# Performance work log

Hardware: AMD Instinct MI355X
Metric: run time of the kernel (lower is better)

The kernel has to match this reference:

```python
import jax, jax.numpy as jnp
import numpy as np

N_STATE = 1024
N_HEAD = 16
B = 2
S = 2048


def setup_inputs() -> dict:
    key = jax.random.key(0)
    ks = jax.random.split(key, 8)
    s = 0.02
    x = jax.random.normal(ks[0], (B, S, N_STATE), dtype=jnp.float32)
    # causal additive mask, as in Whisper: upper triangle = -inf
    mask = jnp.where(jnp.triu(jnp.ones((S, S), dtype=bool), k=1), -jnp.inf, 0.0).astype(jnp.float32)
    Wq = jax.random.normal(ks[1], (N_STATE, N_STATE), dtype=jnp.float32) * s
    bq = jax.random.normal(ks[2], (N_STATE,), dtype=jnp.float32) * s
    Wk = jax.random.normal(ks[3], (N_STATE, N_STATE), dtype=jnp.float32) * s
    Wv = jax.random.normal(ks[4], (N_STATE, N_STATE), dtype=jnp.float32) * s
    bv = jax.random.normal(ks[5], (N_STATE,), dtype=jnp.float32) * s
    Wo = jax.random.normal(ks[6], (N_STATE, N_STATE), dtype=jnp.float32) * s
    bo = jax.random.normal(ks[7], (N_STATE,), dtype=jnp.float32) * s
    return {"x": x, "mask": mask, "Wq": Wq, "bq": bq, "Wk": Wk,
            "Wv": Wv, "bv": bv, "Wo": Wo, "bo": bo}


def reference(x, mask, Wq, bq, Wk, Wv, bv, Wo, bo):
    Bb, S_, D = x.shape
    H = N_HEAD
    hd = D // H
    scale = hd ** (-0.25)  # scale split across q and k, as in the source
    q = x @ Wq.T + bq              # [B,S,D]
    k = x @ Wk.T                   # key has no bias
    v = x @ Wv.T + bv
    # [B,S,D] -> [B,H,S,hd]
    q = q.reshape(Bb, S_, H, hd).transpose(0, 2, 1, 3) * scale
    k = k.reshape(Bb, S_, H, hd).transpose(0, 2, 1, 3) * scale
    v = v.reshape(Bb, S_, H, hd).transpose(0, 2, 1, 3)
    qk = jnp.einsum('bhsd,bhtd->bhst', q, k) + mask[:S_, :S_]
    w = jax.nn.softmax(qk, axis=-1).astype(q.dtype)
    out = jnp.einsum('bhst,bhtd->bhsd', w, v)
    out = out.transpose(0, 2, 1, 3).reshape(Bb, S_, D)
    return out @ Wo.T + bo
```

## Files before the change

kernel.cpp:

```cpp
#include <hip/hip_runtime.h>
#include <hip/hip_bf16.h>
#include <cmath>

typedef __bf16 bf16;
typedef __bf16 bf16x8 __attribute__((ext_vector_type(8)));
typedef __bf16 bf16x4 __attribute__((ext_vector_type(4)));
typedef float f32x4 __attribute__((ext_vector_type(4)));

#define QS 0.18033688f

__device__ __forceinline__ void load16_to_lds(const void* g, void* l) {
    __builtin_amdgcn_global_load_lds(
        (const __attribute__((address_space(1))) unsigned int*)g,
        (__attribute__((address_space(3))) unsigned int*)l, 16, 0, 0);
}

__global__ __launch_bounds__(256) void convert_kernel(
    const float* __restrict__ x,  const float* __restrict__ wq,
    const float* __restrict__ wk, const float* __restrict__ wv,
    const float* __restrict__ wo, bf16* __restrict__ dst)
{
    const size_t M1 = 1024ull * 1024ull, M4 = 4ull * M1;
    size_t i0 = ((size_t)blockIdx.x * 256 + threadIdx.x) * 8;
    const float* s;
    size_t off;
    float sc = 1.f;
    if      (i0 < M4)        { s = x;  off = i0; }
    else if (i0 < M4 + M1)   { s = wq; off = i0 - M4; sc = QS; }
    else if (i0 < M4 + 2*M1) { s = wk; off = i0 - M4 - M1; }
    else if (i0 < M4 + 3*M1) { s = wv; off = i0 - M4 - 2*M1; }
    else                     { s = wo; off = i0 - M4 - 3*M1; }
    float4 a = *(const float4*)(s + off);
    float4 b = *(const float4*)(s + off + 4);
    bf16x8 r = { (bf16)(a.x*sc), (bf16)(a.y*sc), (bf16)(a.z*sc), (bf16)(a.w*sc),
                 (bf16)(b.x*sc), (bf16)(b.y*sc), (bf16)(b.z*sc), (bf16)(b.w*sc) };
    *(bf16x8*)(dst + i0) = r;
}

template<int BM, int MODE>
__device__ __forceinline__ void gemm_core(
    const bf16* __restrict__ A, const bf16* __restrict__ W,
    const float* __restrict__ bias, void* __restrict__ C,
    int mb, int nb, float bias_scale)
{
    constexpr int IF = BM / 32;
    __shared__ __align__(16) bf16 As[BM * 32];
    __shared__ __align__(16) bf16 Bs[128 * 32];

    const int tid  = threadIdx.x;
    const int lane = tid & 63;
    const int wave = tid >> 6;
    const int wr   = (wave >> 1) * (BM / 2);
    const int wc   = (wave & 1) * 64;
    const int l15  = lane & 15;
    const int l4   = lane >> 4;
    const int swz  = (l4 ^ ((l15 >> 1) & 3)) * 8;

    f32x4 acc[IF][4] = {};

    for (int kt = 0; kt < 32; ++kt) {
#pragma unroll
        for (int it = 0; it < BM / 64; ++it) {
            int c = it * 256 + tid;
            int scol = ((c & 3) ^ ((c >> 3) & 3)) * 8;
            load16_to_lds(&A[(size_t)(mb * BM + (c >> 2)) * 1024 + kt * 32 + scol],
                          &As[(it * 256 + (tid & 192)) * 8]);
        }
#pragma unroll
        for (int it = 0; it < 2; ++it) {
            int c = it * 256 + tid;
            int scol = ((c & 3) ^ ((c >> 3) & 3)) * 8;
            load16_to_lds(&W[(size_t)(nb * 128 + (c >> 2)) * 1024 + kt * 32 + scol],
                          &Bs[(it * 256 + (tid & 192)) * 8]);
        }
        __syncthreads();
        bf16x8 af[IF], bfr[4];
#pragma unroll
        for (int i = 0; i < IF; ++i)
            af[i] = *(const bf16x8*)&As[(wr + i * 16 + l15) * 32 + swz];
#pragma unroll
        for (int j = 0; j < 4; ++j)
            bfr[j] = *(const bf16x8*)&Bs[(wc + j * 16 + l15) * 32 + swz];
#pragma unroll
        for (int i = 0; i < IF; ++i)
#pragma unroll
            for (int j = 0; j < 4; ++j)
                acc[i][j] = __builtin_amdgcn_mfma_f32_16x16x32_bf16(
                    af[i], bfr[j], acc[i][j], 0, 0, 0);
        __syncthreads();
    }

    if (MODE == 1 || MODE == 2) {
#pragma unroll
        for (int j = 0; j < 4; ++j) {
            int D = nb * 128 + wc + j * 16 + l15;
            float bv = bias ? bias[D] : 0.f;
            int hh = D >> 6, d = D & 63;
#pragma unroll
            for (int i = 0; i < IF; ++i) {
                int S0 = mb * BM + wr + i * 16 + l4 * 4;
#pragma unroll
                for (int r = 0; r < 4; ++r) {
                    int S = S0 + r;
                    int bb = S >> 11, key = S & 2047;
                    int bh = bb * 16 + hh, nt = key >> 6, ktl = key & 63;
                    size_t idx;
                    if (MODE == 1)
                        idx = ((size_t)(bh * 32 + nt) * 8 + (d >> 5) * 4 + (ktl >> 4)) * 512
                            + ((d >> 3) & 3) * 128 + (ktl & 15) * 8 + (d & 7);
                    else
                        idx = ((size_t)(bh * 32 + nt) * 8 + (ktl >> 5) * 4 + (d >> 4)) * 512
                            + ((ktl >> 3) & 3) * 128 + (d & 15) * 8 + (ktl & 7);
                    ((bf16*)C)[idx] = (bf16)(acc[i][j][r] + bv);
                }
            }
        }
    } else {
#pragma unroll
        for (int j = 0; j < 4; ++j) {
            int col = nb * 128 + wc + j * 16 + l15;
            float bv = bias ? bias[col] * bias_scale : 0.f;
#pragma unroll
            for (int i = 0; i < IF; ++i) {
                int row0 = mb * BM + wr + i * 16 + l4 * 4;
#pragma unroll
                for (int r = 0; r < 4; ++r) {
                    float val = acc[i][j][r] + bv;
                    size_t idx = (size_t)(row0 + r) * 1024 + col;
                    if (MODE == 3) ((float*)C)[idx] = val;
                    else           ((bf16*)C)[idx]  = (bf16)val;
                }
            }
        }
    }
}

__global__ __launch_bounds__(256) void qkv_kernel(
    const bf16* __restrict__ xb,
    const bf16* __restrict__ wqb, const float* __restrict__ bq,
    const bf16* __restrict__ wkb,
    const bf16* __restrict__ wvb, const float* __restrict__ bv,
    bf16* __restrict__ q, bf16* __restrict__ kfb, bf16* __restrict__ vfb)
{
    int mb = blockIdx.x;
    int nbg = blockIdx.y;
    int sel = nbg >> 3, nb = nbg & 7;
    if      (sel == 0) gemm_core<128, 0>(xb, wqb, bq,      q,   mb, nb, QS);
    else if (sel == 1) gemm_core<128, 1>(xb, wkb, nullptr, kfb, mb, nb, 1.f);
    else               gemm_core<128, 2>(xb, wvb, bv,      vfb, mb, nb, 1.f);
}

__global__ __launch_bounds__(256) void oproj_kernel(
    const bf16* __restrict__ ao, const bf16* __restrict__ wob,
    const float* __restrict__ bo, float* __restrict__ out)
{
    gemm_core<128, 3>(ao, wob, bo, out, blockIdx.x, blockIdx.y, 1.f);
}

__global__ __launch_bounds__(64, 4) void attn_kernel(
    const bf16* __restrict__ q, const bf16* __restrict__ kfb,
    const bf16* __restrict__ vfb, bf16* __restrict__ o)
{
    __shared__ __align__(16) bf16 Ps[32 * 72];

    const int lane = threadIdx.x;
    const int l15  = lane & 15;
    const int l4   = lane >> 4;

    const int bh = blockIdx.x;
    const int wt = 63 - blockIdx.y;
    const int b  = bh >> 4, h = bh & 15;
    const int qrow0 = wt * 32;

    bf16x8 qf[2][2];
#pragma unroll
    for (int qb = 0; qb < 2; ++qb)
#pragma unroll
        for (int kk = 0; kk < 2; ++kk)
            qf[qb][kk] = *(const bf16x8*)&q[(size_t)(b * 2048 + qrow0 + qb * 16 + l15) * 1024
                                           + h * 64 + kk * 32 + l4 * 8];

    const bf16* kb = kfb + (size_t)bh * 131072;
    const bf16* vb = vfb + (size_t)bh * 131072;

    f32x4 oacc[2][4] = {};
    float lsum[2] = { 0.f, 0.f };

    const int n = (qrow0 >> 6) + 1;
    for (int nt = 0; nt < n; ++nt) {
        const bf16* kt_ = kb + nt * 4096;
        const bf16* vt_ = vb + nt * 4096;

        f32x4 s[2][4] = {};
#pragma unroll
        for (int kk = 0; kk < 2; ++kk) {
#pragma unroll
            for (int j = 0; j < 4; ++j) {
                bf16x8 kf = *(const bf16x8*)&kt_[(kk * 4 + j) * 512 + lane * 8];
                s[0][j] = __builtin_amdgcn_mfma_f32_16x16x32_bf16(kf, qf[0][kk], s[0][j], 0, 0, 0);
                s[1][j] = __builtin_amdgcn_mfma_f32_16x16x32_bf16(kf, qf[1][kk], s[1][j], 0, 0, 0);
            }
        }

        const bool diag = (nt == n - 1);
#pragma unroll
        for (int qb = 0; qb < 2; ++qb) {
            float pv[4][4];
            if (diag) {
                int qg = qrow0 + qb * 16 + l15;
#pragma unroll
                for (int j = 0; j < 4; ++j)
#pragma unroll
                    for (int r = 0; r < 4; ++r) {
                        int kg = nt * 64 + j * 16 + l4 * 4 + r;
                        pv[j][r] = (kg > qg) ? 0.f : __builtin_amdgcn_exp2f(s[qb][j][r]);
                    }
            } else {
#pragma unroll
                for (int j = 0; j < 4; ++j)
#pragma unroll
                    for (int r = 0; r < 4; ++r)
                        pv[j][r] = __builtin_amdgcn_exp2f(s[qb][j][r]);
            }
#pragma unroll
            for (int j = 0; j < 4; ++j)
                lsum[qb] += (pv[j][0] + pv[j][1]) + (pv[j][2] + pv[j][3]);

#pragma unroll
            for (int j = 0; j < 4; ++j) {
                bf16x4 pk = { (bf16)pv[j][0], (bf16)pv[j][1], (bf16)pv[j][2], (bf16)pv[j][3] };
                *(bf16x4*)&Ps[(qb * 16 + l15) * 72 + j * 16 + l4 * 4] = pk;
            }
        }

#pragma unroll
        for (int kk = 0; kk < 2; ++kk) {
            bf16x8 pf0 = *(const bf16x8*)&Ps[l15 * 72 + kk * 32 + l4 * 8];
            bf16x8 pf1 = *(const bf16x8*)&Ps[(16 + l15) * 72 + kk * 32 + l4 * 8];
#pragma unroll
            for (int f = 0; f < 4; ++f) {
                bf16x8 vf = *(const bf16x8*)&vt_[(kk * 4 + f) * 512 + lane * 8];
                oacc[0][f] = __builtin_amdgcn_mfma_f32_16x16x32_bf16(pf0, vf, oacc[0][f], 0, 0, 0);
                oacc[1][f] = __builtin_amdgcn_mfma_f32_16x16x32_bf16(pf1, vf, oacc[1][f], 0, 0, 0);
            }
        }
    }

#pragma unroll
    for (int qb = 0; qb < 2; ++qb) {
        float ls = lsum[qb];
        ls += __shfl_xor(ls, 16, 64);
        ls += __shfl_xor(ls, 32, 64);
        float rinv[4];
#pragma unroll
        for (int r = 0; r < 4; ++r) rinv[r] = 1.f / __shfl(ls, l4 * 4 + r, 64);
#pragma unroll
        for (int f = 0; f < 4; ++f)
#pragma unroll
            for (int r = 0; r < 4; ++r)
                o[(size_t)(b * 2048 + qrow0 + qb * 16 + l4 * 4 + r) * 1024 + h * 64 + f * 16 + l15]
                    = (bf16)(oacc[qb][f][r] * rinv[r]);
    }
}

extern "C" void kernel_launch(void* const* d_in, const int* in_sizes, int n_in,
                              void* d_out, int out_size, void* d_ws, size_t ws_size,
                              hipStream_t stream)
{
    const float* x  = (const float*)d_in[0];
    const float* Wq = (const float*)d_in[2];
    const float* bq = (const float*)d_in[3];
    const float* Wk = (const float*)d_in[4];
    const float* Wv = (const float*)d_in[5];
    const float* bv = (const float*)d_in[6];
    const float* Wo = (const float*)d_in[7];
    const float* bo = (const float*)d_in[8];
    float* out = (float*)d_out;

    const size_t M1 = 1024ull * 1024ull, M4 = 4ull * M1;
    bf16* base = (bf16*)d_ws;
    bf16* xb  = base;
    bf16* wqb = base + M4;
    bf16* wkb = base + M4 + M1;
    bf16* wvb = base + M4 + 2 * M1;
    bf16* wob = base + M4 + 3 * M1;
    bf16* q   = base + 8 * M1;
    bf16* kfb = base + 12 * M1;
    bf16* vfb = base + 16 * M1;
    bf16* ao  = xb;

    convert_kernel<<<4096, 256, 0, stream>>>(x, Wq, Wk, Wv, Wo, base);
    qkv_kernel<<<dim3(32, 24), 256, 0, stream>>>(xb, wqb, bq, wkb, wvb, bv, q, kfb, vfb);
    attn_kernel<<<dim3(32, 64), 64, 0, stream>>>(q, kfb, vfb, ao);
    oproj_kernel<<<dim3(32, 8), 256, 0, stream>>>(ao, wob, bo, out);
}
```

Baseline: 195.2 us.

## Split causal attention KV loop into chunks and add a combine kernel

The attention kernel gains a third grid dimension that splits each query tile's KV loop into chunks of up to 8 tiles. Chunk partial outputs and row sums go to an fp32 workspace buffer, and a new combine kernel sums them and normalizes. Tiles with only one chunk still write their output directly. The aim is to even out the causal workload imbalance and shorten the tail of long query tiles, at the cost of an extra launch, partial-result memory traffic, and many empty early-exit blocks.

```diff
diff --git a/kernel.cpp b/kernel.cpp
--- a/kernel.cpp
+++ b/kernel.cpp
@@ -159,7 +159,8 @@
 
 __global__ __launch_bounds__(64, 4) void attn_kernel(
     const bf16* __restrict__ q, const bf16* __restrict__ kfb,
-    const bf16* __restrict__ vfb, bf16* __restrict__ o)
+    const bf16* __restrict__ vfb, bf16* __restrict__ o,
+    float* __restrict__ pbuf)
 {
     __shared__ __align__(16) bf16 Ps[32 * 72];
 
@@ -167,10 +168,17 @@
     const int l15  = lane & 15;
     const int l4   = lane >> 4;
 
-    const int bh = blockIdx.x;
-    const int wt = 63 - blockIdx.y;
+    const int bh    = blockIdx.x;
+    const int wt    = 63 - blockIdx.y;
+    const int chunk = blockIdx.z;
     const int b  = bh >> 4, h = bh & 15;
     const int qrow0 = wt * 32;
+
+    const int n   = (wt >> 1) + 1;
+    const int nch = (n + 7) >> 3;
+    if (chunk >= nch) return;
+    const int nt0 = chunk * 8;
+    const int nt1 = (nt0 + 8 < n) ? (nt0 + 8) : n;
 
     bf16x8 qf[2][2];
 #pragma unroll
@@ -186,8 +194,7 @@
     f32x4 oacc[2][4] = {};
     float lsum[2] = { 0.f, 0.f };
 
-    const int n = (qrow0 >> 6) + 1;
-    for (int nt = 0; nt < n; ++nt) {
+    for (int nt = nt0; nt < nt1; ++nt) {
         const bf16* kt_ = kb + nt * 4096;
         const bf16* vt_ = vb + nt * 4096;
 
@@ -246,21 +253,68 @@
         }
     }
 
-#pragma unroll
-    for (int qb = 0; qb < 2; ++qb) {
-        float ls = lsum[qb];
-        ls += __shfl_xor(ls, 16, 64);
-        ls += __shfl_xor(ls, 32, 64);
-        float rinv[4];
-#pragma unroll
-        for (int r = 0; r < 4; ++r) rinv[r] = 1.f / __shfl(ls, l4 * 4 + r, 64);
-#pragma unroll
-        for (int f = 0; f < 4; ++f)
-#pragma unroll
-            for (int r = 0; r < 4; ++r)
-                o[(size_t)(b * 2048 + qrow0 + qb * 16 + l4 * 4 + r) * 1024 + h * 64 + f * 16 + l15]
-                    = (bf16)(oacc[qb][f][r] * rinv[r]);
-    }
+    if (nch == 1) {
+#pragma unroll
+        for (int qb = 0; qb < 2; ++qb) {
+            float ls = lsum[qb];
+            ls += __shfl_xor(ls, 16, 64);
+            ls += __shfl_xor(ls, 32, 64);
+            float rinv[4];
+#pragma unroll
+            for (int r = 0; r < 4; ++r) rinv[r] = 1.f / __shfl(ls, l4 * 4 + r, 64);
+#pragma unroll
+            for (int f = 0; f < 4; ++f)
+#pragma unroll
+                for (int r = 0; r < 4; ++r)
+                    o[(size_t)(b * 2048 + qrow0 + qb * 16 + l4 * 4 + r) * 1024 + h * 64 + f * 16 + l15]
+                        = (bf16)(oacc[qb][f][r] * rinv[r]);
+        }
+    } else {
+        float* ps = pbuf + ((size_t)(bh * 64 + wt) * 4 + chunk) * 2080;
+#pragma unroll
+        for (int qb = 0; qb < 2; ++qb) {
+            float ls = lsum[qb];
+            ls += __shfl_xor(ls, 16, 64);
+            ls += __shfl_xor(ls, 32, 64);
+            if (l4 == 0) ps[2048 + qb * 16 + l15] = ls;
+#pragma unroll
+            for (int f = 0; f < 4; ++f)
+#pragma unroll
+                for (int r = 0; r < 4; ++r)
+                    ps[(qb * 16 + l4 * 4 + r) * 64 + f * 16 + l15] = oacc[qb][f][r];
+        }
+    }
+}
+
+__global__ __launch_bounds__(256) void combine_kernel(
+    const float* __restrict__ pbuf, bf16* __restrict__ ao)
+{
+    const int bh = blockIdx.x;
+    const int wt = 16 + blockIdx.y;
+    const int b = bh >> 4, h = bh & 15;
+    const int n   = (wt >> 1) + 1;
+    const int nch = (n + 7) >> 3;
+
+    const int tid = threadIdx.x;
+    const int qq  = tid >> 3;
+    const int d0  = (tid & 7) * 8;
+
+    const float* base0 = pbuf + (size_t)(bh * 64 + wt) * 4 * 2080;
+
+    float ls = 0.f;
+    float acc[8] = {};
+    for (int c = 0; c < nch; ++c) {
+        const float* p = base0 + c * 2080;
+        ls += p[2048 + qq];
+        float4 a = *(const float4*)(p + qq * 64 + d0);
+        float4 bb = *(const float4*)(p + qq * 64 + d0 + 4);
+        acc[0] += a.x; acc[1] += a.y; acc[2] += a.z; acc[3] += a.w;
+        acc[4] += bb.x; acc[5] += bb.y; acc[6] += bb.z; acc[7] += bb.w;
+    }
+    float inv = 1.f / ls;
+    bf16x8 r = { (bf16)(acc[0]*inv), (bf16)(acc[1]*inv), (bf16)(acc[2]*inv), (bf16)(acc[3]*inv),
+                 (bf16)(acc[4]*inv), (bf16)(acc[5]*inv), (bf16)(acc[6]*inv), (bf16)(acc[7]*inv) };
+    *(bf16x8*)&ao[(size_t)(b * 2048 + wt * 32 + qq) * 1024 + h * 64 + d0] = r;
 }
 
 extern "C" void kernel_launch(void* const* d_in, const int* in_sizes, int n_in,
@@ -288,9 +342,11 @@
     bf16* kfb = base + 12 * M1;
     bf16* vfb = base + 16 * M1;
     bf16* ao  = xb;
+    float* pbuf = (float*)(base + 20 * M1);
 
     convert_kernel<<<4096, 256, 0, stream>>>(x, Wq, Wk, Wv, Wo, base);
     qkv_kernel<<<dim3(32, 24), 256, 0, stream>>>(xb, wqb, bq, wkb, wvb, bv, q, kfb, vfb);
-    attn_kernel<<<dim3(32, 64), 64, 0, stream>>>(q, kfb, vfb, ao);
+    attn_kernel<<<dim3(32, 64, 4), 64, 0, stream>>>(q, kfb, vfb, ao, pbuf);
+    combine_kernel<<<dim3(32, 48), 256, 0, stream>>>(pbuf, ao);
     oproj_kernel<<<dim3(32, 8), 256, 0, stream>>>(ao, wob, bo, out);
 }
```

Result: slower. 211.0 us (+8.1%).
